# Kernel optimization log

Hardware: AMD Instinct MI355X
Metric: run time of the kernel (lower is better)

The kernel has to match this reference:

```python
import jax, jax.numpy as jnp
import numpy as np

ATT = 256
NUM_GENES = 2128
HIDDEN = 512
B, T = 128, 1024


def setup_inputs() -> dict:
    key = jax.random.key(0)
    ks = jax.random.split(key, 8)
    return {
        "genes": jax.random.normal(ks[0], (B, NUM_GENES), dtype=jnp.float32),
        "smiles": jax.random.normal(ks[1], (B, T, HIDDEN), dtype=jnp.float32),
        "w_num_gene_features": jax.random.normal(ks[2], (1,), dtype=jnp.float32) * 0.1,
        "w_genes": jax.random.normal(ks[3], (NUM_GENES, ATT), dtype=jnp.float32) * 0.1,
        "b_genes": jax.random.normal(ks[4], (ATT,), dtype=jnp.float32) * 0.1,
        "dense_kernel": jax.random.normal(ks[5], (HIDDEN, ATT), dtype=jnp.float32) * 0.05,
        "dense_bias": jnp.zeros((ATT,), dtype=jnp.float32),
        "v": jax.random.normal(ks[6], (ATT,), dtype=jnp.float32) * 0.1,
    }


def reference(genes, smiles, w_num_gene_features, w_genes, b_genes,
              dense_kernel, dense_bias, v):
    # genes: [B, G]; collapse trivial feature axis via scalar weight -> [B, G]
    genes_collapsed = genes * w_num_gene_features[0]
    # gene context: [B, A]
    gene_proj = genes_collapsed @ w_genes + b_genes
    # smiles projection: [B, T, A]
    smiles_proj = jnp.einsum('bth,ha->bta', smiles, dense_kernel) + dense_bias
    # additive attention energies
    x = jnp.tanh(gene_proj[:, None, :] + smiles_proj)          # [B, T, A]
    xv = jnp.einsum('bta,a->bt', x, v)                          # [B, T]
    alphas = jax.nn.softmax(xv, axis=-1)                        # [B, T]
    output = jnp.einsum('bth,bt->bh', smiles, alphas)           # [B, H]
    return output, alphas
```

## Files before the change

### kernel.cpp

```cpp
#include <hip/hip_runtime.h>
#include <stdint.h>

#define B_ 128
#define T_ 1024
#define H_ 512
#define A_ 256
#define G_ 2128

typedef short s16x8 __attribute__((ext_vector_type(8)));
typedef float f32x4 __attribute__((ext_vector_type(4)));
typedef unsigned int u32;

__device__ inline unsigned short f2bf(float f) {
  unsigned u = __float_as_uint(f);
  u += 0x7fff + ((u >> 16) & 1);
  return (unsigned short)(u >> 16);
}
__device__ inline unsigned pack2bf(float a, float b) {
  return ((unsigned)f2bf(b) << 16) | f2bf(a);
}
__device__ inline float fast_tanh(float x) {
  x = fminf(15.f, fmaxf(-15.f, x));
  float e = __expf(2.f * x);
  return (e - 1.f) * __builtin_amdgcn_rcpf(e + 1.f);
}
__device__ inline void gl_lds16(const void* g, void* l) {
  __builtin_amdgcn_global_load_lds(
      (const __attribute__((address_space(1))) u32*)g,
      (__attribute__((address_space(3))) u32*)l, 16, 0, 0);
}

__global__ void prep_kt(const float* __restrict__ K,
                        unsigned short* __restrict__ khi) {
  int idx = blockIdx.x * 256 + threadIdx.x;
  int h = idx >> 8;
  int a = idx & 255;
  int kb = h >> 5, k = h & 31;
  int grp = k >> 3, sub = k & 7;
  khi[kb * 8192 + a * 32 + ((grp ^ (a & 3)) * 8) + sub] = f2bf(K[idx]);
}

__global__ __launch_bounds__(256) void gene_proj_k(
    const float* __restrict__ genes, const float* __restrict__ w0p,
    const float* __restrict__ Wg, const float* __restrict__ bg,
    const float* __restrict__ db, float* __restrict__ gp4) {
  __shared__ float sg[532];
  int b = blockIdx.x;
  int gc = blockIdx.y;
  int a = threadIdx.x;
  int g0 = gc * 532;
  for (int i = threadIdx.x; i < 532; i += 256) sg[i] = genes[(size_t)b * G_ + g0 + i];
  __syncthreads();
  float s = 0.f;
  #pragma unroll 8
  for (int g = 0; g < 532; ++g)
    s = fmaf(sg[g], Wg[(size_t)(g0 + g) * A_ + a], s);
  float val = w0p[0] * s;
  if (gc == 0) val += bg[a] + db[a];
  gp4[(gc * B_ + b) * A_ + a] = val;
}

__global__ __launch_bounds__(256, 3) void fused1(
    const float* __restrict__ smiles, const unsigned short* __restrict__ khi,
    const float* __restrict__ gp4, const float* __restrict__ v,
    float* __restrict__ xv, float* __restrict__ ml, float* __restrict__ outp) {
  __shared__ unsigned short sA[64 * 32];
  __shared__ unsigned short sB[256 * 32];
  __shared__ float sXV[64 * 4];
  __shared__ float sP[64];

  const int tid = threadIdx.x;
  const int b = blockIdx.y;
  const int tb = blockIdx.x;
  const int lane = tid & 63;
  const int w = tid >> 6;
  const int n = lane & 15;
  const int q = lane >> 4;

  const int ar = tid >> 2;
  const int g8 = tid & 3;
  const int s0 = (g8 ^ (ar & 3)) * 8;
  const float* asrc = smiles + ((size_t)(b * 1024 + tb * 64 + ar)) * 512 + g8 * 8;

  f32x4 acc[4][4];
  #pragma unroll
  for (int i = 0; i < 4; ++i)
    #pragma unroll
    for (int j = 0; j < 4; ++j)
      acc[i][j] = (f32x4){0.f, 0.f, 0.f, 0.f};

  float4 f0 = *reinterpret_cast<const float4*>(asrc);
  float4 f1 = *reinterpret_cast<const float4*>(asrc + 4);

  for (int kb = 0; kb < 16; ++kb) {
    __builtin_amdgcn_sched_barrier(0);
    __builtin_amdgcn_s_barrier();
    __builtin_amdgcn_sched_barrier(0);

    uint4 p0;
    p0.x = pack2bf(f0.x, f0.y); p0.y = pack2bf(f0.z, f0.w);
    p0.z = pack2bf(f1.x, f1.y); p0.w = pack2bf(f1.z, f1.w);
    *reinterpret_cast<uint4*>(&sA[ar * 32 + s0]) = p0;
    __builtin_amdgcn_sched_barrier(0);
    #pragma unroll
    for (int r = 0; r < 4; ++r)
      gl_lds16(khi + kb * 8192 + w * 2048 + r * 512 + lane * 8,
               &sB[w * 2048 + r * 512]);
    __builtin_amdgcn_sched_barrier(0);
    {
      int noff = (kb < 15) ? (kb + 1) * 32 : 0;
      f0 = *reinterpret_cast<const float4*>(asrc + noff);
      f1 = *reinterpret_cast<const float4*>(asrc + noff + 4);
    }
    asm volatile("s_waitcnt vmcnt(2) lgkmcnt(0)" ::: "memory");
    __builtin_amdgcn_sched_barrier(0);
    __builtin_amdgcn_s_barrier();
    __builtin_amdgcn_sched_barrier(0);

    s16x8 af[4], bh[4];
    const int sw = (q ^ (n & 3)) * 8;
    #pragma unroll
    for (int j = 0; j < 4; ++j)
      bh[j] = *reinterpret_cast<const s16x8*>(&sB[(w * 64 + j * 16 + n) * 32 + sw]);
    #pragma unroll
    for (int i = 0; i < 4; ++i)
      af[i] = *reinterpret_cast<const s16x8*>(&sA[(i * 16 + n) * 32 + sw]);
    #pragma unroll
    for (int i = 0; i < 4; ++i)
      #pragma unroll
      for (int j = 0; j < 4; ++j)
        acc[i][j] = __builtin_amdgcn_mfma_f32_16x16x32_bf16(af[i], bh[j], acc[i][j], 0, 0, 0);
  }

  float vv[4], gg[4];
  #pragma unroll
  for (int j = 0; j < 4; ++j) {
    int a = w * 64 + j * 16 + n;
    int idx = b * A_ + a;
    vv[j] = v[a];
    gg[j] = gp4[idx] + gp4[B_ * A_ + idx] + gp4[2 * B_ * A_ + idx] +
            gp4[3 * B_ * A_ + idx];
  }
  #pragma unroll
  for (int i = 0; i < 4; ++i) {
    #pragma unroll
    for (int r = 0; r < 4; ++r) {
      float s = 0.f;
      #pragma unroll
      for (int j = 0; j < 4; ++j)
        s += vv[j] * fast_tanh(acc[i][j][r] + gg[j]);
      s += __shfl_xor(s, 1); s += __shfl_xor(s, 2);
      s += __shfl_xor(s, 4); s += __shfl_xor(s, 8);
      if (n == 0) sXV[(i * 16 + q * 4 + r) * 4 + w] = s;
    }
  }
  __syncthreads();

  if (w == 0) {
    float* p = &sXV[lane * 4];
    float xvv = p[0] + p[1] + p[2] + p[3];
    xv[(size_t)b * T_ + tb * 64 + lane] = xvv;
    float mx = xvv;
    #pragma unroll
    for (int o = 1; o < 64; o <<= 1) mx = fmaxf(mx, __shfl_xor(mx, o));
    float e = __expf(xvv - mx);
    sP[lane] = e;
    float lsum = e;
    #pragma unroll
    for (int o = 1; o < 64; o <<= 1) lsum += __shfl_xor(lsum, o);
    if (lane == 0) {
      ml[(b * 16 + tb) * 2] = mx;
      ml[(b * 16 + tb) * 2 + 1] = lsum;
    }
  }
  __syncthreads();

  float2 a2 = {0.f, 0.f};
  const float* sm2 = smiles + ((size_t)(b * 1024 + tb * 64)) * 512 + tid * 2;
  #pragma unroll 8
  for (int t = 0; t < 64; ++t) {
    float a = sP[t];
    float2 sv = *reinterpret_cast<const float2*>(sm2 + (size_t)t * 512);
    a2.x = fmaf(a, sv.x, a2.x);
    a2.y = fmaf(a, sv.y, a2.y);
  }
  *reinterpret_cast<float2*>(outp + ((size_t)(b * 16 + tb)) * 512 + tid * 2) = a2;
}

__global__ __launch_bounds__(256) void merge_k(
    const float* __restrict__ ml, const float* __restrict__ outp,
    const float* __restrict__ xv, float* __restrict__ out,
    float* __restrict__ alphas) {
  int b = blockIdx.x, tid = threadIdx.x;
  float m[16], lq[16];
  float M = -1e30f;
  #pragma unroll
  for (int t = 0; t < 16; ++t) {
    m[t] = ml[(b * 16 + t) * 2];
    lq[t] = ml[(b * 16 + t) * 2 + 1];
    M = fmaxf(M, m[t]);
  }
  float L = 0.f, wq[16];
  #pragma unroll
  for (int t = 0; t < 16; ++t) {
    wq[t] = __expf(m[t] - M);
    L = fmaf(lq[t], wq[t], L);
  }
  float invL = 1.f / L;
  float2 o2 = {0.f, 0.f};
  #pragma unroll
  for (int t = 0; t < 16; ++t) {
    float2 p = *reinterpret_cast<const float2*>(outp + ((size_t)(b * 16 + t)) * 512 + tid * 2);
    o2.x = fmaf(wq[t], p.x, o2.x);
    o2.y = fmaf(wq[t], p.y, o2.y);
  }
  o2.x *= invL; o2.y *= invL;
  *reinterpret_cast<float2*>(out + (size_t)b * H_ + tid * 2) = o2;
  #pragma unroll
  for (int t = tid; t < T_; t += 256)
    alphas[(size_t)b * T_ + t] = __expf(xv[(size_t)b * T_ + t] - M) * invL;
}

extern "C" void kernel_launch(void* const* d_in, const int* in_sizes, int n_in,
                              void* d_out, int out_size, void* d_ws, size_t ws_size,
                              hipStream_t stream) {
  const float* genes  = (const float*)d_in[0];
  const float* smiles = (const float*)d_in[1];
  const float* w0     = (const float*)d_in[2];
  const float* wg     = (const float*)d_in[3];
  const float* bg     = (const float*)d_in[4];
  const float* dk     = (const float*)d_in[5];
  const float* db     = (const float*)d_in[6];
  const float* v      = (const float*)d_in[7];
  float* out = (float*)d_out;
  char* ws = (char*)d_ws;
  float* gp4 = (float*)ws;
  unsigned short* khi = (unsigned short*)(ws + 524288);
  float* xv   = (float*)(ws + 786432);
  float* ml   = (float*)(ws + 1310720);
  float* outp = (float*)(ws + 1327104);
  float* alphas = out + B_ * H_;

  prep_kt<<<512, 256, 0, stream>>>(dk, khi);
  gene_proj_k<<<dim3(B_, 4), 256, 0, stream>>>(genes, w0, wg, bg, db, gp4);
  fused1<<<dim3(16, B_), 256, 0, stream>>>(smiles, khi, gp4, v, xv, ml, outp);
  merge_k<<<B_, 256, 0, stream>>>(ml, outp, xv, out, alphas);
}
```

Baseline: 476.2 us.

## Double-buffer LDS tiles in fused projection GEMM to overlap loads with MFMA

The shared A (smiles, converted to bf16) and B (dense kernel) tiles become ping-pong buffers. The next k-block's LDS writes and global_load_lds are issued before the current block's MFMAs, so only one barrier per iteration is needed. The goal is to hide global and LDS load latency behind the MFMA work instead of stalling at a barrier before every compute step. In exchange it roughly doubles the tile LDS footprint and depends on hand-placed waitcnt ordering being correct.

```diff
diff --git a/kernel.cpp b/kernel.cpp
--- a/kernel.cpp
+++ b/kernel.cpp
@@ -64,8 +64,8 @@
     const float* __restrict__ smiles, const unsigned short* __restrict__ khi,
     const float* __restrict__ gp4, const float* __restrict__ v,
     float* __restrict__ xv, float* __restrict__ ml, float* __restrict__ outp) {
-  __shared__ unsigned short sA[64 * 32];
-  __shared__ unsigned short sB[256 * 32];
+  __shared__ unsigned short sA[2][64 * 32];
+  __shared__ unsigned short sB[2][256 * 32];
   __shared__ float sXV[64 * 4];
   __shared__ float sP[64];
 
@@ -91,45 +91,61 @@
 
   float4 f0 = *reinterpret_cast<const float4*>(asrc);
   float4 f1 = *reinterpret_cast<const float4*>(asrc + 4);
-
-  for (int kb = 0; kb < 16; ++kb) {
-    __builtin_amdgcn_sched_barrier(0);
-    __builtin_amdgcn_s_barrier();
-    __builtin_amdgcn_sched_barrier(0);
-
+  {
     uint4 p0;
     p0.x = pack2bf(f0.x, f0.y); p0.y = pack2bf(f0.z, f0.w);
     p0.z = pack2bf(f1.x, f1.y); p0.w = pack2bf(f1.z, f1.w);
-    *reinterpret_cast<uint4*>(&sA[ar * 32 + s0]) = p0;
-    __builtin_amdgcn_sched_barrier(0);
+    *reinterpret_cast<uint4*>(&sA[0][ar * 32 + s0]) = p0;
     #pragma unroll
     for (int r = 0; r < 4; ++r)
-      gl_lds16(khi + kb * 8192 + w * 2048 + r * 512 + lane * 8,
-               &sB[w * 2048 + r * 512]);
-    __builtin_amdgcn_sched_barrier(0);
-    {
-      int noff = (kb < 15) ? (kb + 1) * 32 : 0;
+      gl_lds16(khi + w * 2048 + r * 512 + lane * 8, &sB[0][w * 2048 + r * 512]);
+    f0 = *reinterpret_cast<const float4*>(asrc + 32);
+    f1 = *reinterpret_cast<const float4*>(asrc + 32 + 4);
+    asm volatile("s_waitcnt lgkmcnt(0)" ::: "memory");
+    __builtin_amdgcn_sched_barrier(0);
+    __builtin_amdgcn_s_barrier();
+    __builtin_amdgcn_sched_barrier(0);
+  }
+
+  const int sw = (q ^ (n & 3)) * 8;
+  for (int kb = 0; kb < 16; ++kb) {
+    const int cur = kb & 1;
+    const int nxt = cur ^ 1;
+    asm volatile("s_waitcnt vmcnt(2)" ::: "memory");
+    __builtin_amdgcn_sched_barrier(0);
+
+    s16x8 af[4], bh[4];
+    #pragma unroll
+    for (int j = 0; j < 4; ++j)
+      bh[j] = *reinterpret_cast<const s16x8*>(&sB[cur][(w * 64 + j * 16 + n) * 32 + sw]);
+    #pragma unroll
+    for (int i = 0; i < 4; ++i)
+      af[i] = *reinterpret_cast<const s16x8*>(&sA[cur][(i * 16 + n) * 32 + sw]);
+
+    if (kb < 15) {
+      uint4 p0;
+      p0.x = pack2bf(f0.x, f0.y); p0.y = pack2bf(f0.z, f0.w);
+      p0.z = pack2bf(f1.x, f1.y); p0.w = pack2bf(f1.z, f1.w);
+      *reinterpret_cast<uint4*>(&sA[nxt][ar * 32 + s0]) = p0;
+      #pragma unroll
+      for (int r = 0; r < 4; ++r)
+        gl_lds16(khi + (kb + 1) * 8192 + w * 2048 + r * 512 + lane * 8,
+                 &sB[nxt][w * 2048 + r * 512]);
+      int noff = (kb < 14) ? (kb + 2) * 32 : 15 * 32;
       f0 = *reinterpret_cast<const float4*>(asrc + noff);
       f1 = *reinterpret_cast<const float4*>(asrc + noff + 4);
     }
-    asm volatile("s_waitcnt vmcnt(2) lgkmcnt(0)" ::: "memory");
-    __builtin_amdgcn_sched_barrier(0);
-    __builtin_amdgcn_s_barrier();
-    __builtin_amdgcn_sched_barrier(0);
-
-    s16x8 af[4], bh[4];
-    const int sw = (q ^ (n & 3)) * 8;
-    #pragma unroll
-    for (int j = 0; j < 4; ++j)
-      bh[j] = *reinterpret_cast<const s16x8*>(&sB[(w * 64 + j * 16 + n) * 32 + sw]);
-    #pragma unroll
-    for (int i = 0; i < 4; ++i)
-      af[i] = *reinterpret_cast<const s16x8*>(&sA[(i * 16 + n) * 32 + sw]);
+
     #pragma unroll
     for (int i = 0; i < 4; ++i)
       #pragma unroll
       for (int j = 0; j < 4; ++j)
         acc[i][j] = __builtin_amdgcn_mfma_f32_16x16x32_bf16(af[i], bh[j], acc[i][j], 0, 0, 0);
+
+    asm volatile("s_waitcnt lgkmcnt(0)" ::: "memory");
+    __builtin_amdgcn_sched_barrier(0);
+    __builtin_amdgcn_s_barrier();
+    __builtin_amdgcn_sched_barrier(0);
   }
 
   float vv[4], gg[4];
```

After: 482.2 us. No clear change (+1.3%).
